# Performance work log

Measured on AMD Instinct MI355X. Metric: run time of the kernel, lower is better.

Reference implementation:

```python
import jax, jax.numpy as jnp
import numpy as np


def setup_inputs() -> dict:
    key = jax.random.key(0)
    k1, k2, k3 = jax.random.split(key, 3)
    B, S_TOT, HD = 2, 4096, 1024
    return {
        "q": jax.random.normal(k1, (B, S_TOT, HD), dtype=jnp.float32),
        "k": jax.random.normal(k2, (B, S_TOT, HD), dtype=jnp.float32),
        "v": jax.random.normal(k3, (B, S_TOT, HD), dtype=jnp.float32),
        "num_heads": 16,
        "num_shots": 4,
        "per_g": 64,
    }


def reference(q, k, v, num_heads, num_shots, per_g):
    # Equal-length shots: shot_latent_indices = [0, L, 2L, ..., s_tot] per batch.
    b, s_tot, hd = q.shape
    d = hd // num_heads
    L = s_tot // num_shots  # local shot length
    scale = 1.0 / jnp.sqrt(jnp.asarray(d, q.dtype))

    # [b, S, L, H, D]
    qs = q.reshape(b, num_shots, L, num_heads, d)
    ks = k.reshape(b, num_shots, L, num_heads, d)
    vs = v.reshape(b, num_shots, L, num_heads, d)

    # Global pool: first per_g tokens of each shot ('firstk'), shared by all shots.
    kg = ks[:, :, :per_g].reshape(b, num_shots * per_g, num_heads, d)  # [b, G, H, D]
    vg = vs[:, :, :per_g].reshape(b, num_shots * per_g, num_heads, d)

    # Block-local scores [b,S,H,L,L] and shared-global scores [b,S,H,L,G]
    s_loc = jnp.einsum("bsqhd,bskhd->bshqk", qs, ks) * scale
    s_glb = jnp.einsum("bsqhd,bghd->bshqg", qs, kg) * scale
    logits = jnp.concatenate([s_loc, s_glb], axis=-1)  # [b,S,H,L,L+G]
    p = jax.nn.softmax(logits, axis=-1)

    o_loc = jnp.einsum("bshqk,bskhd->bsqhd", p[..., :L], vs)
    o_glb = jnp.einsum("bshqg,bghd->bsqhd", p[..., L:], vg)
    out = (o_loc + o_glb).reshape(b, s_tot, hd)
    return out
```

## Files before the change

kernel.cpp:

```cpp
#include <hip/hip_runtime.h>
#include <hip/hip_bf16.h>

#define S_TOT 4096
#define HDIM  1024
#define NH    16
#define DH    64
#define L_    1024
#define NT_LOC 16
#define NT_TOT 20

using bf16x8 = __attribute__((ext_vector_type(8))) short;
using f32x16 = __attribute__((ext_vector_type(16))) float;
using i32x4  = __attribute__((ext_vector_type(4))) int;

typedef const __attribute__((address_space(1))) unsigned int* gp1_t;
typedef __attribute__((address_space(3))) unsigned int* lp3_t;

__device__ __forceinline__ short f2bf(float f) {
    union { float f; unsigned u; } x; x.f = f;
    unsigned r = x.u + 0x7FFFu + ((x.u >> 16) & 1u);
    return (short)(r >> 16);
}

__device__ __forceinline__ unsigned cvt_pk_bf16(float lo, float hi) {
    unsigned r;
    asm("v_cvt_pk_bf16_f32 %0, %1, %2" : "=v"(r) : "v"(lo), "v"(hi));
    return r;
}

__device__ __forceinline__ float exp2_fast(float x) {
#if __has_builtin(__builtin_amdgcn_exp2f)
    return __builtin_amdgcn_exp2f(x);
#else
    return exp2f(x);
#endif
}

__device__ __forceinline__ void gload16(const void* g, void* l) {
    __builtin_amdgcn_global_load_lds((gp1_t)g, (lp3_t)(unsigned long)(l), 16, 0, 0);
}

__global__ __launch_bounds__(256) void prep_kv(
    const float* __restrict__ kf, const float* __restrict__ vf,
    short* __restrict__ kb, short* __restrict__ vb)
{
    __shared__ short st[64 * 70];
    const int bid = blockIdx.x, tid = threadIdx.x;
    if (bid < 1024) {
        const int gid = bid * 256 + tid;
        #pragma unroll
        for (int it = 0; it < 2; ++it) {
            size_t e = ((size_t)gid + (size_t)it * 262144) * 16;
            #pragma unroll
            for (int half = 0; half < 2; ++half) {
                float4 a = *(const float4*)(kf + e + half * 8);
                float4 c = *(const float4*)(kf + e + half * 8 + 4);
                bf16x8 r;
                r[0]=f2bf(a.x); r[1]=f2bf(a.y); r[2]=f2bf(a.z); r[3]=f2bf(a.w);
                r[4]=f2bf(c.x); r[5]=f2bf(c.y); r[6]=f2bf(c.z); r[7]=f2bf(c.w);
                *(bf16x8*)(kb + e + half * 8) = r;
            }
        }
    } else {
        const int vbid = bid - 1024;
        const int stile = vbid & 63, ht = (vbid >> 6) & 15, b = vbid >> 10;
        const int rt = tid >> 2, q4 = tid & 3;
        const float* src = vf + ((size_t)(b * S_TOT + stile * 64 + rt)) * HDIM + ht * 64 + q4 * 16;
        short* dst = st + rt * 70 + q4 * 16;
        #pragma unroll
        for (int i = 0; i < 4; ++i) {
            float4 x = *(const float4*)(src + i * 4);
            dst[i*4+0] = f2bf(x.x); dst[i*4+1] = f2bf(x.y);
            dst[i*4+2] = f2bf(x.z); dst[i*4+3] = f2bf(x.w);
        }
        __syncthreads();
        const int orow = tid >> 2, oq = tid & 3;
        bf16x8 o0, o1;
        #pragma unroll
        for (int j = 0; j < 8; ++j) o0[j] = st[(oq * 16 + j) * 70 + orow];
        #pragma unroll
        for (int j = 0; j < 8; ++j) o1[j] = st[(oq * 16 + 8 + j) * 70 + orow];
        short* dst2 = vb + ((size_t)((b * NH + ht) * 64 + orow)) * S_TOT + stile * 64 + oq * 16;
        *(bf16x8*)dst2 = o0;
        *(bf16x8*)(dst2 + 8) = o1;
    }
}

__global__ __launch_bounds__(512, 4) void attn_kernel(
    const float* __restrict__ qf, const short* __restrict__ kb,
    const short* __restrict__ vb, float* __restrict__ out)
{
    __shared__ __align__(16) char smem[32768];
    const int tid  = threadIdx.x;
    const int wave = tid >> 6, lane = tid & 63;
    const int hi   = lane >> 5, q32 = lane & 31;

    const int bidhw = blockIdx.x;
    const int bid = ((bidhw & 7) << 6) | (bidhw >> 3);
    const int qt = bid & 3, h = (bid >> 2) & 15, s = (bid >> 6) & 3, b = bid >> 8;

    const float CSC = 0.125f * 1.4426950408889634f;
    const float* qp = qf + ((size_t)(b*S_TOT + s*L_ + qt*256 + wave*32 + q32)) * HDIM
                         + h * DH + hi * 8;
    bf16x8 qv[4];
    #pragma unroll
    for (int d = 0; d < 4; ++d) {
        float4 x0 = *(const float4*)(qp + d * 16);
        float4 x1 = *(const float4*)(qp + d * 16 + 4);
        i32x4 u;
        u[0] = (int)cvt_pk_bf16(x0.x * CSC, x0.y * CSC);
        u[1] = (int)cvt_pk_bf16(x0.z * CSC, x0.w * CSC);
        u[2] = (int)cvt_pk_bf16(x1.x * CSC, x1.y * CSC);
        u[3] = (int)cvt_pk_bf16(x1.z * CSC, x1.w * CSC);
        qv[d] = __builtin_bit_cast(bf16x8, u);
    }

    const int cid = wave * 64 + lane;
    const int row = cid >> 3;
    const int lch = (cid & 7) ^ (row & 7);
    const int krow = (row & 0x33) | ((row & 4) << 1) | ((row & 8) >> 1);
    const size_t ko = (size_t)krow * 2048 + (lch << 4);
    const size_t vo = (size_t)row  * 8192 + (lch << 4);
    const char* kbase = (const char*)kb + ((size_t)b * S_TOT) * 2048 + h * 128;
    const char* vbase = (const char*)vb + ((size_t)(b * NH + h)) * (64ull * 8192);

    auto stage = [&](int tt, int bufo) {
        const int abs_tile = (tt < NT_LOC) ? (s * NT_LOC + tt) : ((tt - NT_LOC) * NT_LOC);
        const char* kp = kbase + (size_t)abs_tile * (64 * 2048);
        const char* vp = vbase + (size_t)abs_tile * 128;
        char* dK = smem + bufo + wave * 1024;
        gload16(kp + ko, dK);
        gload16(vp + vo, dK + 8192);
    };

    int qc[4];
    #pragma unroll
    for (int i = 0; i < 4; ++i)
        qc[i] = q32 * 128 + (((i * 2 + hi) ^ (q32 & 7)) << 4);

    f32x16 zro;
    #pragma unroll
    for (int r = 0; r < 16; ++r) zro[r] = 0.f;
    f32x16 acc0 = zro, acc1 = zro;
    float ps = 0.f;

    const char* sb = smem;
    stage(0, 0);

    #define TILE_ITER(T, BUFO) do {                                              \
        if ((T) + 1 < NT_TOT) {                                                  \
            stage((T) + 1, (BUFO) ^ 16384);                                      \
            asm volatile("s_waitcnt vmcnt(2)" ::: "memory");                     \
        } else {                                                                 \
            asm volatile("s_waitcnt vmcnt(0)" ::: "memory");                     \
        }                                                                        \
        __builtin_amdgcn_sched_barrier(0);                                       \
        __builtin_amdgcn_s_barrier();                                            \
        __builtin_amdgcn_sched_barrier(0);                                       \
        f32x16 sA, sB;                                                           \
        {                                                                        \
            __builtin_amdgcn_s_setprio(1);                                       \
            bf16x8 a0 = *(const bf16x8*)(sb + (BUFO) + qc[0]);                   \
            bf16x8 b0 = *(const bf16x8*)(sb + (BUFO) + 4096 + qc[0]);            \
            sA = __builtin_amdgcn_mfma_f32_32x32x16_bf16(a0, qv[0], zro,0,0,0);  \
            sB = __builtin_amdgcn_mfma_f32_32x32x16_bf16(b0, qv[0], zro,0,0,0);  \
            bf16x8 a1 = *(const bf16x8*)(sb + (BUFO) + qc[1]);                   \
            bf16x8 b1 = *(const bf16x8*)(sb + (BUFO) + 4096 + qc[1]);            \
            sA = __builtin_amdgcn_mfma_f32_32x32x16_bf16(a1, qv[1], sA,0,0,0);   \
            sB = __builtin_amdgcn_mfma_f32_32x32x16_bf16(b1, qv[1], sB,0,0,0);   \
            bf16x8 a2 = *(const bf16x8*)(sb + (BUFO) + qc[2]);                   \
            bf16x8 b2 = *(const bf16x8*)(sb + (BUFO) + 4096 + qc[2]);            \
            sA = __builtin_amdgcn_mfma_f32_32x32x16_bf16(a2, qv[2], sA,0,0,0);   \
            sB = __builtin_amdgcn_mfma_f32_32x32x16_bf16(b2, qv[2], sB,0,0,0);   \
            bf16x8 a3 = *(const bf16x8*)(sb + (BUFO) + qc[3]);                   \
            bf16x8 b3 = *(const bf16x8*)(sb + (BUFO) + 4096 + qc[3]);            \
            sA = __builtin_amdgcn_mfma_f32_32x32x16_bf16(a3, qv[3], sA,0,0,0);   \
            sB = __builtin_amdgcn_mfma_f32_32x32x16_bf16(b3, qv[3], sB,0,0,0);   \
            __builtin_amdgcn_s_setprio(0);                                       \
        }                                                                        \
        _Pragma("unroll")                                                        \
        for (int r = 0; r < 16; ++r) {                                           \
            float p = exp2_fast(sA[r]); sA[r] = p; ps += p;                      \
        }                                                                        \
        _Pragma("unroll")                                                        \
        for (int r = 0; r < 16; ++r) {                                           \
            float p = exp2_fast(sB[r]); sB[r] = p; ps += p;                      \
        }                                                                        \
        bf16x8 pf0, pf1, pf2, pf3;                                               \
        {   i32x4 u;                                                             \
            u[0]=(int)cvt_pk_bf16(sA[0],sA[1]);  u[1]=(int)cvt_pk_bf16(sA[2],sA[3]);   \
            u[2]=(int)cvt_pk_bf16(sA[4],sA[5]);  u[3]=(int)cvt_pk_bf16(sA[6],sA[7]);   \
            pf0 = __builtin_bit_cast(bf16x8, u);                                 \
            u[0]=(int)cvt_pk_bf16(sA[8],sA[9]);  u[1]=(int)cvt_pk_bf16(sA[10],sA[11]); \
            u[2]=(int)cvt_pk_bf16(sA[12],sA[13]);u[3]=(int)cvt_pk_bf16(sA[14],sA[15]); \
            pf1 = __builtin_bit_cast(bf16x8, u);                                 \
            u[0]=(int)cvt_pk_bf16(sB[0],sB[1]);  u[1]=(int)cvt_pk_bf16(sB[2],sB[3]);   \
            u[2]=(int)cvt_pk_bf16(sB[4],sB[5]);  u[3]=(int)cvt_pk_bf16(sB[6],sB[7]);   \
            pf2 = __builtin_bit_cast(bf16x8, u);                                 \
            u[0]=(int)cvt_pk_bf16(sB[8],sB[9]);  u[1]=(int)cvt_pk_bf16(sB[10],sB[11]); \
            u[2]=(int)cvt_pk_bf16(sB[12],sB[13]);u[3]=(int)cvt_pk_bf16(sB[14],sB[15]); \
            pf3 = __builtin_bit_cast(bf16x8, u);                                 \
        }                                                                        \
        {                                                                        \
            __builtin_amdgcn_s_setprio(1);                                       \
            bf16x8 v00 = *(const bf16x8*)(sb + (BUFO) + 8192 + qc[0]);           \
            bf16x8 v10 = *(const bf16x8*)(sb + (BUFO) + 12288 + qc[0]);          \
            acc0 = __builtin_amdgcn_mfma_f32_32x32x16_bf16(v00, pf0, acc0,0,0,0);\
            acc1 = __builtin_amdgcn_mfma_f32_32x32x16_bf16(v10, pf0, acc1,0,0,0);\
            bf16x8 v01 = *(const bf16x8*)(sb + (BUFO) + 8192 + qc[1]);           \
            bf16x8 v11 = *(const bf16x8*)(sb + (BUFO) + 12288 + qc[1]);          \
            acc0 = __builtin_amdgcn_mfma_f32_32x32x16_bf16(v01, pf1, acc0,0,0,0);\
            acc1 = __builtin_amdgcn_mfma_f32_32x32x16_bf16(v11, pf1, acc1,0,0,0);\
            bf16x8 v02 = *(const bf16x8*)(sb + (BUFO) + 8192 + qc[2]);           \
            bf16x8 v12 = *(const bf16x8*)(sb + (BUFO) + 12288 + qc[2]);          \
            acc0 = __builtin_amdgcn_mfma_f32_32x32x16_bf16(v02, pf2, acc0,0,0,0);\
            acc1 = __builtin_amdgcn_mfma_f32_32x32x16_bf16(v12, pf2, acc1,0,0,0);\
            bf16x8 v03 = *(const bf16x8*)(sb + (BUFO) + 8192 + qc[3]);           \
            bf16x8 v13 = *(const bf16x8*)(sb + (BUFO) + 12288 + qc[3]);          \
            acc0 = __builtin_amdgcn_mfma_f32_32x32x16_bf16(v03, pf3, acc0,0,0,0);\
            acc1 = __builtin_amdgcn_mfma_f32_32x32x16_bf16(v13, pf3, acc1,0,0,0);\
            __builtin_amdgcn_s_setprio(0);                                       \
        }                                                                        \
        asm volatile("s_waitcnt lgkmcnt(0)" ::: "memory");                       \
        __builtin_amdgcn_sched_barrier(0);                                       \
        __builtin_amdgcn_s_barrier();                                            \
        __builtin_amdgcn_sched_barrier(0);                                       \
    } while (0)

    for (int t = 0; t < NT_TOT; t += 2) {
        TILE_ITER(t, 0);
        TILE_ITER(t + 1, 16384);
    }
    #undef TILE_ITER

    float tot = ps + __shfl_xor(ps, 32);
    float inv = 1.0f / tot;
    const size_t orow = (size_t)(b*S_TOT + s*L_ + qt*256 + wave*32 + q32);
    float* op = out + orow * HDIM + h * DH;
    #pragma unroll
    for (int m = 0; m < 4; ++m) {
        float4 w0, w1;
        w0.x = acc0[4*m+0]*inv; w0.y = acc0[4*m+1]*inv;
        w0.z = acc0[4*m+2]*inv; w0.w = acc0[4*m+3]*inv;
        *(float4*)(op + 8*m + 4*hi) = w0;
        w1.x = acc1[4*m+0]*inv; w1.y = acc1[4*m+1]*inv;
        w1.z = acc1[4*m+2]*inv; w1.w = acc1[4*m+3]*inv;
        *(float4*)(op + 32 + 8*m + 4*hi) = w1;
    }
}

extern "C" void kernel_launch(void* const* d_in, const int* in_sizes, int n_in,
                              void* d_out, int out_size, void* d_ws, size_t ws_size,
                              hipStream_t stream) {
    const float* q = (const float*)d_in[0];
    const float* k = (const float*)d_in[1];
    const float* v = (const float*)d_in[2];
    char* ws = (char*)d_ws;
    short* kbuf = (short*)(ws);
    short* vbuf = (short*)(ws + (16u << 20));
    prep_kv<<<dim3(3072), dim3(256), 0, stream>>>(k, v, kbuf, vbuf);
    attn_kernel<<<dim3(512), dim3(512), 0, stream>>>(q, kbuf, vbuf, (float*)d_out);
}
```

Measured before the change: 73.76 us.

## Give each wave two query subtiles and fold the duplicate own-shot global tile into local

Blocks shrink from 8 to 4 waves, and each wave now handles 64 query rows as two 32-row subtiles. Each K/V fragment read from LDS therefore feeds twice as many MFMAs, and each thread issues four async global loads per tile instead of two. The global tile that duplicates the first local tile of the block's own shot is no longer loaded. Its double weight is recovered by adding 1 to the exponent on tile 0, which cuts the loop from 20 to 19 tiles. The cost is higher register pressure and fewer waves per CU to hide latency.

```diff
diff --git a/kernel.cpp b/kernel.cpp
--- a/kernel.cpp
+++ b/kernel.cpp
@@ -6,8 +6,7 @@
 #define NH    16
 #define DH    64
 #define L_    1024
-#define NT_LOC 16
-#define NT_TOT 20
+#define NT    19
 
 using bf16x8 = __attribute__((ext_vector_type(8))) short;
 using f32x16 = __attribute__((ext_vector_type(16))) float;
@@ -86,7 +85,7 @@
     }
 }
 
-__global__ __launch_bounds__(512, 4) void attn_kernel(
+__global__ __launch_bounds__(256, 2) void attn_kernel(
     const float* __restrict__ qf, const short* __restrict__ kb,
     const short* __restrict__ vb, float* __restrict__ out)
 {
@@ -100,23 +99,25 @@
     const int qt = bid & 3, h = (bid >> 2) & 15, s = (bid >> 6) & 3, b = bid >> 8;
 
     const float CSC = 0.125f * 1.4426950408889634f;
-    const float* qp = qf + ((size_t)(b*S_TOT + s*L_ + qt*256 + wave*32 + q32)) * HDIM
-                         + h * DH + hi * 8;
-    bf16x8 qv[4];
-    #pragma unroll
-    for (int d = 0; d < 4; ++d) {
-        float4 x0 = *(const float4*)(qp + d * 16);
-        float4 x1 = *(const float4*)(qp + d * 16 + 4);
-        i32x4 u;
-        u[0] = (int)cvt_pk_bf16(x0.x * CSC, x0.y * CSC);
-        u[1] = (int)cvt_pk_bf16(x0.z * CSC, x0.w * CSC);
-        u[2] = (int)cvt_pk_bf16(x1.x * CSC, x1.y * CSC);
-        u[3] = (int)cvt_pk_bf16(x1.z * CSC, x1.w * CSC);
-        qv[d] = __builtin_bit_cast(bf16x8, u);
-    }
-
-    const int cid = wave * 64 + lane;
-    const int row = cid >> 3;
+    bf16x8 qv[2][4];
+    #pragma unroll
+    for (int qs = 0; qs < 2; ++qs) {
+        const float* qp = qf + ((size_t)(b*S_TOT + s*L_ + qt*256 + wave*64 + qs*32 + q32)) * HDIM
+                             + h * DH + hi * 8;
+        #pragma unroll
+        for (int d = 0; d < 4; ++d) {
+            float4 x0 = *(const float4*)(qp + d * 16);
+            float4 x1 = *(const float4*)(qp + d * 16 + 4);
+            i32x4 u;
+            u[0] = (int)cvt_pk_bf16(x0.x * CSC, x0.y * CSC);
+            u[1] = (int)cvt_pk_bf16(x0.z * CSC, x0.w * CSC);
+            u[2] = (int)cvt_pk_bf16(x1.x * CSC, x1.y * CSC);
+            u[3] = (int)cvt_pk_bf16(x1.z * CSC, x1.w * CSC);
+            qv[qs][d] = __builtin_bit_cast(bf16x8, u);
+        }
+    }
+
+    const int cid = tid, row = cid >> 3;
     const int lch = (cid & 7) ^ (row & 7);
     const int krow = (row & 0x33) | ((row & 4) << 1) | ((row & 8) >> 1);
     const size_t ko = (size_t)krow * 2048 + (lch << 4);
@@ -124,13 +125,20 @@
     const char* kbase = (const char*)kb + ((size_t)b * S_TOT) * 2048 + h * 128;
     const char* vbase = (const char*)vb + ((size_t)(b * NH + h)) * (64ull * 8192);
 
-    auto stage = [&](int tt, int bufo) {
-        const int abs_tile = (tt < NT_LOC) ? (s * NT_LOC + tt) : ((tt - NT_LOC) * NT_LOC);
-        const char* kp = kbase + (size_t)abs_tile * (64 * 2048);
-        const char* vp = vbase + (size_t)abs_tile * 128;
-        char* dK = smem + bufo + wave * 1024;
-        gload16(kp + ko, dK);
-        gload16(vp + vo, dK + 8192);
+    auto abs_tile_of = [&](int t) -> int {
+        if (t < 16) return s * 16 + t;
+        int g = t - 16; if (g >= s) ++g;
+        return g * 16;
+    };
+    auto stage = [&](int t, int bo) {
+        const int at = abs_tile_of(t);
+        const char* kp = kbase + (size_t)at * 131072;
+        const char* vp = vbase + (size_t)at * 128;
+        char* dst = smem + bo + wave * 1024;
+        gload16(kp + ko,          dst);
+        gload16(kp + ko + 65536,  dst + 4096);
+        gload16(vp + vo,          dst + 8192);
+        gload16(vp + vo + 262144, dst + 12288);
     };
 
     int qc[4];
@@ -141,111 +149,118 @@
     f32x16 zro;
     #pragma unroll
     for (int r = 0; r < 16; ++r) zro[r] = 0.f;
-    f32x16 acc0 = zro, acc1 = zro;
-    float ps = 0.f;
-
-    const char* sb = smem;
+    f32x16 acc[2][2];
+    acc[0][0] = zro; acc[0][1] = zro; acc[1][0] = zro; acc[1][1] = zro;
+    float ps[2] = {0.f, 0.f};
+
     stage(0, 0);
-
-    #define TILE_ITER(T, BUFO) do {                                              \
-        if ((T) + 1 < NT_TOT) {                                                  \
-            stage((T) + 1, (BUFO) ^ 16384);                                      \
-            asm volatile("s_waitcnt vmcnt(2)" ::: "memory");                     \
-        } else {                                                                 \
-            asm volatile("s_waitcnt vmcnt(0)" ::: "memory");                     \
-        }                                                                        \
-        __builtin_amdgcn_sched_barrier(0);                                       \
-        __builtin_amdgcn_s_barrier();                                            \
-        __builtin_amdgcn_sched_barrier(0);                                       \
-        f32x16 sA, sB;                                                           \
-        {                                                                        \
-            __builtin_amdgcn_s_setprio(1);                                       \
-            bf16x8 a0 = *(const bf16x8*)(sb + (BUFO) + qc[0]);                   \
-            bf16x8 b0 = *(const bf16x8*)(sb + (BUFO) + 4096 + qc[0]);            \
-            sA = __builtin_amdgcn_mfma_f32_32x32x16_bf16(a0, qv[0], zro,0,0,0);  \
-            sB = __builtin_amdgcn_mfma_f32_32x32x16_bf16(b0, qv[0], zro,0,0,0);  \
-            bf16x8 a1 = *(const bf16x8*)(sb + (BUFO) + qc[1]);                   \
-            bf16x8 b1 = *(const bf16x8*)(sb + (BUFO) + 4096 + qc[1]);            \
-            sA = __builtin_amdgcn_mfma_f32_32x32x16_bf16(a1, qv[1], sA,0,0,0);   \
-            sB = __builtin_amdgcn_mfma_f32_32x32x16_bf16(b1, qv[1], sB,0,0,0);   \
-            bf16x8 a2 = *(const bf16x8*)(sb + (BUFO) + qc[2]);                   \
-            bf16x8 b2 = *(const bf16x8*)(sb + (BUFO) + 4096 + qc[2]);            \
-            sA = __builtin_amdgcn_mfma_f32_32x32x16_bf16(a2, qv[2], sA,0,0,0);   \
-            sB = __builtin_amdgcn_mfma_f32_32x32x16_bf16(b2, qv[2], sB,0,0,0);   \
-            bf16x8 a3 = *(const bf16x8*)(sb + (BUFO) + qc[3]);                   \
-            bf16x8 b3 = *(const bf16x8*)(sb + (BUFO) + 4096 + qc[3]);            \
-            sA = __builtin_amdgcn_mfma_f32_32x32x16_bf16(a3, qv[3], sA,0,0,0);   \
-            sB = __builtin_amdgcn_mfma_f32_32x32x16_bf16(b3, qv[3], sB,0,0,0);   \
-            __builtin_amdgcn_s_setprio(0);                                       \
-        }                                                                        \
-        _Pragma("unroll")                                                        \
-        for (int r = 0; r < 16; ++r) {                                           \
-            float p = exp2_fast(sA[r]); sA[r] = p; ps += p;                      \
-        }                                                                        \
-        _Pragma("unroll")                                                        \
-        for (int r = 0; r < 16; ++r) {                                           \
-            float p = exp2_fast(sB[r]); sB[r] = p; ps += p;                      \
-        }                                                                        \
-        bf16x8 pf0, pf1, pf2, pf3;                                               \
-        {   i32x4 u;                                                             \
-            u[0]=(int)cvt_pk_bf16(sA[0],sA[1]);  u[1]=(int)cvt_pk_bf16(sA[2],sA[3]);   \
-            u[2]=(int)cvt_pk_bf16(sA[4],sA[5]);  u[3]=(int)cvt_pk_bf16(sA[6],sA[7]);   \
-            pf0 = __builtin_bit_cast(bf16x8, u);                                 \
-            u[0]=(int)cvt_pk_bf16(sA[8],sA[9]);  u[1]=(int)cvt_pk_bf16(sA[10],sA[11]); \
-            u[2]=(int)cvt_pk_bf16(sA[12],sA[13]);u[3]=(int)cvt_pk_bf16(sA[14],sA[15]); \
-            pf1 = __builtin_bit_cast(bf16x8, u);                                 \
-            u[0]=(int)cvt_pk_bf16(sB[0],sB[1]);  u[1]=(int)cvt_pk_bf16(sB[2],sB[3]);   \
-            u[2]=(int)cvt_pk_bf16(sB[4],sB[5]);  u[3]=(int)cvt_pk_bf16(sB[6],sB[7]);   \
-            pf2 = __builtin_bit_cast(bf16x8, u);                                 \
-            u[0]=(int)cvt_pk_bf16(sB[8],sB[9]);  u[1]=(int)cvt_pk_bf16(sB[10],sB[11]); \
-            u[2]=(int)cvt_pk_bf16(sB[12],sB[13]);u[3]=(int)cvt_pk_bf16(sB[14],sB[15]); \
-            pf3 = __builtin_bit_cast(bf16x8, u);                                 \
-        }                                                                        \
-        {                                                                        \
-            __builtin_amdgcn_s_setprio(1);                                       \
-            bf16x8 v00 = *(const bf16x8*)(sb + (BUFO) + 8192 + qc[0]);           \
-            bf16x8 v10 = *(const bf16x8*)(sb + (BUFO) + 12288 + qc[0]);          \
-            acc0 = __builtin_amdgcn_mfma_f32_32x32x16_bf16(v00, pf0, acc0,0,0,0);\
-            acc1 = __builtin_amdgcn_mfma_f32_32x32x16_bf16(v10, pf0, acc1,0,0,0);\
-            bf16x8 v01 = *(const bf16x8*)(sb + (BUFO) + 8192 + qc[1]);           \
-            bf16x8 v11 = *(const bf16x8*)(sb + (BUFO) + 12288 + qc[1]);          \
-            acc0 = __builtin_amdgcn_mfma_f32_32x32x16_bf16(v01, pf1, acc0,0,0,0);\
-            acc1 = __builtin_amdgcn_mfma_f32_32x32x16_bf16(v11, pf1, acc1,0,0,0);\
-            bf16x8 v02 = *(const bf16x8*)(sb + (BUFO) + 8192 + qc[2]);           \
-            bf16x8 v12 = *(const bf16x8*)(sb + (BUFO) + 12288 + qc[2]);          \
-            acc0 = __builtin_amdgcn_mfma_f32_32x32x16_bf16(v02, pf2, acc0,0,0,0);\
-            acc1 = __builtin_amdgcn_mfma_f32_32x32x16_bf16(v12, pf2, acc1,0,0,0);\
-            bf16x8 v03 = *(const bf16x8*)(sb + (BUFO) + 8192 + qc[3]);           \
-            bf16x8 v13 = *(const bf16x8*)(sb + (BUFO) + 12288 + qc[3]);          \
-            acc0 = __builtin_amdgcn_mfma_f32_32x32x16_bf16(v03, pf3, acc0,0,0,0);\
-            acc1 = __builtin_amdgcn_mfma_f32_32x32x16_bf16(v13, pf3, acc1,0,0,0);\
-            __builtin_amdgcn_s_setprio(0);                                       \
-        }                                                                        \
-        asm volatile("s_waitcnt lgkmcnt(0)" ::: "memory");                       \
-        __builtin_amdgcn_sched_barrier(0);                                       \
-        __builtin_amdgcn_s_barrier();                                            \
-        __builtin_amdgcn_sched_barrier(0);                                       \
-    } while (0)
-
-    for (int t = 0; t < NT_TOT; t += 2) {
-        TILE_ITER(t, 0);
-        TILE_ITER(t + 1, 16384);
-    }
-    #undef TILE_ITER
-
-    float tot = ps + __shfl_xor(ps, 32);
-    float inv = 1.0f / tot;
-    const size_t orow = (size_t)(b*S_TOT + s*L_ + qt*256 + wave*32 + q32);
-    float* op = out + orow * HDIM + h * DH;
-    #pragma unroll
-    for (int m = 0; m < 4; ++m) {
-        float4 w0, w1;
-        w0.x = acc0[4*m+0]*inv; w0.y = acc0[4*m+1]*inv;
-        w0.z = acc0[4*m+2]*inv; w0.w = acc0[4*m+3]*inv;
-        *(float4*)(op + 8*m + 4*hi) = w0;
-        w1.x = acc1[4*m+0]*inv; w1.y = acc1[4*m+1]*inv;
-        w1.z = acc1[4*m+2]*inv; w1.w = acc1[4*m+3]*inv;
-        *(float4*)(op + 32 + 8*m + 4*hi) = w1;
+    int bufo = 0;
+    for (int t = 0; t < NT; ++t) {
+        if (t + 1 < NT) {
+            stage(t + 1, bufo ^ 16384);
+            asm volatile("s_waitcnt vmcnt(4)" ::: "memory");
+        } else {
+            asm volatile("s_waitcnt vmcnt(0)" ::: "memory");
+        }
+        __builtin_amdgcn_sched_barrier(0);
+        __builtin_amdgcn_s_barrier();
+        __builtin_amdgcn_sched_barrier(0);
+        const char* sb = smem + bufo;
+
+        #pragma unroll
+        for (int half = 0; half < 2; ++half) {
+            const int koff = half * 4096;
+            f32x16 S[2];
+            __builtin_amdgcn_s_setprio(1);
+            bf16x8 f0 = *(const bf16x8*)(sb + koff + qc[0]);
+            bf16x8 f1 = *(const bf16x8*)(sb + koff + qc[1]);
+            bf16x8 f2 = *(const bf16x8*)(sb + koff + qc[2]);
+            bf16x8 f3 = *(const bf16x8*)(sb + koff + qc[3]);
+            #pragma unroll
+            for (int qs = 0; qs < 2; ++qs) {
+                f32x16 a = __builtin_amdgcn_mfma_f32_32x32x16_bf16(f0, qv[qs][0], zro, 0,0,0);
+                a = __builtin_amdgcn_mfma_f32_32x32x16_bf16(f1, qv[qs][1], a, 0,0,0);
+                a = __builtin_amdgcn_mfma_f32_32x32x16_bf16(f2, qv[qs][2], a, 0,0,0);
+                a = __builtin_amdgcn_mfma_f32_32x32x16_bf16(f3, qv[qs][3], a, 0,0,0);
+                S[qs] = a;
+            }
+            __builtin_amdgcn_s_setprio(0);
+
+            if (t == 0) {
+                #pragma unroll
+                for (int qs = 0; qs < 2; ++qs)
+                    #pragma unroll
+                    for (int r = 0; r < 16; ++r)
+                        S[qs][r] = exp2_fast(S[qs][r] + 1.0f);
+            } else {
+                #pragma unroll
+                for (int qs = 0; qs < 2; ++qs)
+                    #pragma unroll
+                    for (int r = 0; r < 16; ++r)
+                        S[qs][r] = exp2_fast(S[qs][r]);
+            }
+            #pragma unroll
+            for (int qs = 0; qs < 2; ++qs) {
+                float s0 = (S[qs][0] + S[qs][1]) + (S[qs][2] + S[qs][3]);
+                float s1 = (S[qs][4] + S[qs][5]) + (S[qs][6] + S[qs][7]);
+                float s2 = (S[qs][8] + S[qs][9]) + (S[qs][10] + S[qs][11]);
+                float s3 = (S[qs][12] + S[qs][13]) + (S[qs][14] + S[qs][15]);
+                ps[qs] += (s0 + s1) + (s2 + s3);
+            }
+
+            bf16x8 pf[2][2];
+            #pragma unroll
+            for (int qs = 0; qs < 2; ++qs) {
+                i32x4 u;
+                u[0] = (int)cvt_pk_bf16(S[qs][0],  S[qs][1]);
+                u[1] = (int)cvt_pk_bf16(S[qs][2],  S[qs][3]);
+                u[2] = (int)cvt_pk_bf16(S[qs][4],  S[qs][5]);
+                u[3] = (int)cvt_pk_bf16(S[qs][6],  S[qs][7]);
+                pf[qs][0] = __builtin_bit_cast(bf16x8, u);
+                u[0] = (int)cvt_pk_bf16(S[qs][8],  S[qs][9]);
+                u[1] = (int)cvt_pk_bf16(S[qs][10], S[qs][11]);
+                u[2] = (int)cvt_pk_bf16(S[qs][12], S[qs][13]);
+                u[3] = (int)cvt_pk_bf16(S[qs][14], S[qs][15]);
+                pf[qs][1] = __builtin_bit_cast(bf16x8, u);
+            }
+
+            __builtin_amdgcn_s_setprio(1);
+            bf16x8 w00 = *(const bf16x8*)(sb + 8192  + qc[2*half]);
+            bf16x8 w01 = *(const bf16x8*)(sb + 8192  + qc[2*half+1]);
+            bf16x8 w10 = *(const bf16x8*)(sb + 12288 + qc[2*half]);
+            bf16x8 w11 = *(const bf16x8*)(sb + 12288 + qc[2*half+1]);
+            #pragma unroll
+            for (int qs = 0; qs < 2; ++qs) {
+                acc[qs][0] = __builtin_amdgcn_mfma_f32_32x32x16_bf16(w00, pf[qs][0], acc[qs][0], 0,0,0);
+                acc[qs][0] = __builtin_amdgcn_mfma_f32_32x32x16_bf16(w01, pf[qs][1], acc[qs][0], 0,0,0);
+                acc[qs][1] = __builtin_amdgcn_mfma_f32_32x32x16_bf16(w10, pf[qs][0], acc[qs][1], 0,0,0);
+                acc[qs][1] = __builtin_amdgcn_mfma_f32_32x32x16_bf16(w11, pf[qs][1], acc[qs][1], 0,0,0);
+            }
+            __builtin_amdgcn_s_setprio(0);
+        }
+
+        __builtin_amdgcn_sched_barrier(0);
+        __builtin_amdgcn_s_barrier();
+        __builtin_amdgcn_sched_barrier(0);
+        bufo ^= 16384;
+    }
+
+    #pragma unroll
+    for (int qs = 0; qs < 2; ++qs) {
+        float tot = ps[qs] + __shfl_xor(ps[qs], 32);
+        float inv = 1.0f / tot;
+        const size_t orow = (size_t)(b*S_TOT + s*L_ + qt*256 + wave*64 + qs*32 + q32);
+        float* op = out + orow * HDIM + h * DH;
+        #pragma unroll
+        for (int m = 0; m < 4; ++m) {
+            float4 w0, w1;
+            w0.x = acc[qs][0][4*m+0]*inv; w0.y = acc[qs][0][4*m+1]*inv;
+            w0.z = acc[qs][0][4*m+2]*inv; w0.w = acc[qs][0][4*m+3]*inv;
+            *(float4*)(op + 8*m + 4*hi) = w0;
+            w1.x = acc[qs][1][4*m+0]*inv; w1.y = acc[qs][1][4*m+1]*inv;
+            w1.z = acc[qs][1][4*m+2]*inv; w1.w = acc[qs][1][4*m+3]*inv;
+            *(float4*)(op + 32 + 8*m + 4*hi) = w1;
+        }
     }
 }
 
@@ -259,5 +274,5 @@
     short* kbuf = (short*)(ws);
     short* vbuf = (short*)(ws + (16u << 20));
     prep_kv<<<dim3(3072), dim3(256), 0, stream>>>(k, v, kbuf, vbuf);
-    attn_kernel<<<dim3(512), dim3(512), 0, stream>>>(q, kbuf, vbuf, (float*)d_out);
-}
+    attn_kernel<<<dim3(512), dim3(256), 0, stream>>>(q, kbuf, vbuf, (float*)d_out);
+}
```

New measurement: 71.22 us. -3.4%, faster.
